# Kernel tuning notes

Measured on AMD Instinct MI355X. Metric: run time of the kernel, lower is better.

The kernel has to match this reference:

```python
import jax, jax.numpy as jnp
import numpy as np

NMS_THR = 0.7
TOPK = 128      # fixed post-NMS rois per level (static padding for jit)
OUT = 14        # RoIAlign output size
SAMPLES = 2     # samples per bin per dim (fixed approximation of sampling_ratio=-1)
STRIDES = (32.0, 16.0, 8.0)


def get_channel(a):
    # a: [..., 4] boxes as (cx, cy, w, h); FPN level assignment, clamped to [1, 4]
    s = jnp.sqrt(a[..., 2] * a[..., 3])
    return jnp.clip(jnp.floor(3.0 + jnp.log2(s / 224.0)), 1.0, 4.0)


def cxcywh_to_xyxy(b):
    cx, cy, w, h = b[..., 0], b[..., 1], b[..., 2], b[..., 3]
    return jnp.stack([cx - w / 2, cy - h / 2, cx + w / 2, cy + h / 2], axis=-1)


def pairwise_iou(b):
    x1, y1, x2, y2 = b[:, 0], b[:, 1], b[:, 2], b[:, 3]
    area = jnp.maximum(x2 - x1, 0.0) * jnp.maximum(y2 - y1, 0.0)
    ix1 = jnp.maximum(x1[:, None], x1[None, :])
    iy1 = jnp.maximum(y1[:, None], y1[None, :])
    ix2 = jnp.minimum(x2[:, None], x2[None, :])
    iy2 = jnp.minimum(y2[:, None], y2[None, :])
    inter = jnp.maximum(ix2 - ix1, 0.0) * jnp.maximum(iy2 - iy1, 0.0)
    union = area[:, None] + area[None, :] - inter
    return inter / jnp.maximum(union, 1e-9)


def nms_keep(boxes_xyxy, scores, thr):
    # Greedy NMS over masked scores (-inf entries sort last and are excluded later).
    n = scores.shape[0]
    order = jnp.argsort(-scores)
    iou = pairwise_iou(boxes_xyxy[order])  # [N, N]
    idx = jnp.arange(n)

    def body(sup, i):
        keep_i = ~sup[i]
        sup = sup | (keep_i & (iou[i] > thr) & (idx > i))
        return sup, keep_i

    _, keeps_sorted = jax.lax.scan(body, jnp.zeros(n, dtype=bool), idx)
    return jnp.zeros(n, dtype=bool).at[order].set(keeps_sorted)


def roi_align(feat, boxes):
    # feat: [C, H, W]; boxes: [K, 4]. NOTE: the original prepare_boxes feeds
    # (cx, cy, w, h) straight into RoIAlign, which interprets them as
    # (x1, y1, x2, y2) -- replicated faithfully here. spatial_scale = 1.
    C, H, W = feat.shape
    K = boxes.shape[0]
    x1, y1, x2, y2 = boxes[:, 0], boxes[:, 1], boxes[:, 2], boxes[:, 3]
    rw = jnp.maximum(x2 - x1, 1.0)
    rh = jnp.maximum(y2 - y1, 1.0)
    bw = rw / OUT
    bh = rh / OUT
    # fractional bin offsets, [OUT*SAMPLES]
    f = (jnp.arange(OUT, dtype=feat.dtype)[:, None]
         + (jnp.arange(SAMPLES, dtype=feat.dtype)[None, :] + 0.5) / SAMPLES).reshape(-1)
    ys = y1[:, None] + bh[:, None] * f[None, :]  # [K, S]
    xs = x1[:, None] + bw[:, None] * f[None, :]
    Y = ys[:, :, None]  # [K, S, 1]
    X = xs[:, None, :]  # [K, 1, S]
    valid = (Y > -1.0) & (Y < H) & (X > -1.0) & (X < W)  # [K, S, S]
    Yc = jnp.clip(Y, 0.0, H - 1.0)
    Xc = jnp.clip(X, 0.0, W - 1.0)
    y0 = jnp.floor(Yc)
    x0 = jnp.floor(Xc)
    y0i = y0.astype(jnp.int32)
    x0i = x0.astype(jnp.int32)
    y1i = jnp.minimum(y0i + 1, H - 1)
    x1i = jnp.minimum(x0i + 1, W - 1)
    ly = Yc - y0
    lx = Xc - x0
    hy = 1.0 - ly
    hx = 1.0 - lx
    g = lambda yi, xi: feat[:, yi, xi]  # -> [C, K, S, S]
    val = (g(y0i, x0i) * (hy * hx) + g(y0i, x1i) * (hy * lx)
           + g(y1i, x0i) * (ly * hx) + g(y1i, x1i) * (ly * lx))
    val = val * valid.astype(val.dtype)
    val = val.reshape(C, K, OUT, SAMPLES, OUT, SAMPLES).mean(axis=(3, 5))
    return jnp.transpose(val, (1, 0, 2, 3))  # [K, C, OUT, OUT]


def level_extract(feat, boxes, scores, levs, nl):
    # one image, one target FPN level: mask, NMS, fixed top-K select, RoIAlign
    mask = levs == nl
    msc = jnp.where(mask, scores, -jnp.inf)
    xyxy = cxcywh_to_xyxy(boxes)
    keep = nms_keep(jax.lax.stop_gradient(xyxy), jax.lax.stop_gradient(msc), NMS_THR)
    eff = jnp.where(keep & mask, msc, -jnp.inf)
    vals, sel = jax.lax.top_k(jax.lax.stop_gradient(eff), TOPK)
    valid = jnp.isfinite(vals)
    rois = boxes[sel] * valid[:, None].astype(boxes.dtype)
    out = roi_align(feat, rois)
    return out * valid[:, None, None, None].astype(out.dtype)


def _forward(p32, p16, p8, p4, a32, a16, a8, s32, s16, s8):
    anchors = (a32, a16, a8)  # p4 proposals are computed then discarded in the
    # original (grouping loop only runs l in range(3)); p4 features are never
    # RoIAligned either (nl loops 1..3), so p4 only appears as an unused input.
    levs = jnp.concatenate([get_channel(a) for a in anchors], axis=1)      # [B, N]
    boxes = jnp.concatenate([a * s for a, s in zip(anchors, STRIDES)], axis=1)
    scores = jnp.concatenate([s32, s16, s8], axis=1)
    outs = []
    for nl, feat in zip((1.0, 2.0, 3.0), (p32, p16, p8)):
        fn = jax.vmap(lambda f, b, s, l, nl=nl: level_extract(f, b, s, l, nl))
        outs.append(fn(feat, boxes, scores, levs))  # [B, TOPK, C, 14, 14]
    return jnp.concatenate(outs, axis=1)  # [B, 3*TOPK, C, 14, 14]


def setup_inputs():
    key = jax.random.key(0)
    ks = jax.random.split(key, 10)
    B, C = 2, 256
    p32 = jax.random.normal(ks[0], (B, C, 32, 32), jnp.float32)
    p16 = jax.random.normal(ks[1], (B, C, 64, 64), jnp.float32)
    p8 = jax.random.normal(ks[2], (B, C, 128, 128), jnp.float32)
    p4 = jax.random.normal(ks[3], (B, C, 256, 256), jnp.float32)

    def mk_anchors(k, n, hf):
        k1, k2 = jax.random.split(k)
        cxy = jax.random.uniform(k1, (B, n, 2), jnp.float32) * hf
        wh = 16.0 + jax.random.uniform(k2, (B, n, 2), jnp.float32) * 434.0
        return jnp.concatenate([cxy, wh], axis=-1)

    anchors_32 = mk_anchors(ks[4], 512, 32.0)
    anchors_16 = mk_anchors(ks[5], 1024, 64.0)
    anchors_8 = mk_anchors(ks[6], 2048, 128.0)
    scores_32 = jax.random.normal(ks[7], (B, 512), jnp.float32)
    scores_16 = jax.random.normal(ks[8], (B, 1024), jnp.float32)
    scores_8 = jax.random.normal(ks[9], (B, 2048), jnp.float32)
    return dict(p32=p32, p16=p16, p8=p8, p4=p4,
                anchors_32=anchors_32, anchors_16=anchors_16, anchors_8=anchors_8,
                scores_32=scores_32, scores_16=scores_16, scores_8=scores_8)


def reference(p32, p16, p8, p4, anchors_32, anchors_16, anchors_8,
              scores_32, scores_16, scores_8):
    return _forward(p32, p16, p8, p4, anchors_32, anchors_16, anchors_8,
                    scores_32, scores_16, scores_8)
```

## Files before the change

### kernel.cpp

```cpp
#include <hip/hip_runtime.h>
#include <stdint.h>

#define NMS_THR 0.7f
#define TOPK 128
#define NTOT 3584
#define CAP 2048
#define CHUNK 256
#define OUTSZ 14
#define NSAMP 28

typedef unsigned long long u64;
typedef float vf4 __attribute__((ext_vector_type(4)));
typedef float float2u __attribute__((ext_vector_type(2), aligned(4)));

__device__ __forceinline__ u64 shfl_xor64(u64 v, int mask) {
    int lo = __shfl_xor((int)(unsigned)v, mask);
    int hi = __shfl_xor((int)(v >> 32), mask);
    return ((u64)(unsigned)hi << 32) | (unsigned)lo;
}
__device__ __forceinline__ void cex_shfl(u64 &e, int t, int j, int k) {
    u64 p = shfl_xor64(e, j);
    bool up = ((t & k) == 0);
    bool lower = ((t & j) == 0);
    u64 mn = (e < p) ? e : p;
    u64 mx = (e < p) ? p : e;
    e = (lower == up) ? mn : mx;
}
__device__ __forceinline__ float boxarea(float4 b) {
    return __fmul_rn(fmaxf(__fsub_rn(b.z, b.x), 0.0f),
                     fmaxf(__fsub_rn(b.w, b.y), 0.0f));
}
__device__ __forceinline__ bool iou_gt(float4 a, float aa, float4 b, float ba) {
    float i1 = fmaxf(a.x, b.x), i2 = fmaxf(a.y, b.y);
    float i3 = fminf(a.z, b.z), i4 = fminf(a.w, b.w);
    float inr = __fmul_rn(fmaxf(__fsub_rn(i3, i1), 0.0f),
                          fmaxf(__fsub_rn(i4, i2), 0.0f));
    float unr = __fsub_rn(__fadd_rn(aa, ba), inr);
    return __fdiv_rn(inr, fmaxf(unr, 1e-9f)) > NMS_THR;
}

__device__ __forceinline__ void fetch_anchor(
    const float* __restrict__ a32, const float* __restrict__ a16,
    const float* __restrict__ a8,
    const float* __restrict__ s32, const float* __restrict__ s16,
    const float* __restrict__ s8,
    int b, int i, float* A, float* st, float* sc)
{
    const float* P;
    if (i < 512) {
        P = a32 + (b * 512 + i) * 4;  *st = 32.0f; *sc = s32[b * 512 + i];
    } else if (i < 1536) {
        int j = i - 512;
        P = a16 + (b * 1024 + j) * 4; *st = 16.0f; *sc = s16[b * 1024 + j];
    } else {
        int j = i - 1536;
        P = a8 + (b * 2048 + j) * 4;  *st = 8.0f;  *sc = s8[b * 2048 + j];
    }
    float4 v = *(const float4*)P;
    A[0] = v.x; A[1] = v.y; A[2] = v.z; A[3] = v.w;
}

__global__ __launch_bounds__(1024) void select_kernel(
    const float* __restrict__ a32, const float* __restrict__ a16,
    const float* __restrict__ a8,
    const float* __restrict__ s32, const float* __restrict__ s16,
    const float* __restrict__ s8,
    float* __restrict__ rois,
    int* __restrict__ validOut)
{
    __shared__ u64 keys[CAP];
    __shared__ float4 cbox4[CAP];
    __shared__ float4 kb4[TOPK];
    __shared__ float karea[TOPK];
    __shared__ u64 extw[16];
    __shared__ int selList[TOPK];
    __shared__ int mCount, keptSh;

    int prob = blockIdx.x;
    int b = prob / 3;
    int nl = prob % 3 + 1;
    int tid = threadIdx.x;
    int lane = tid & 63;
    int wv = tid >> 6;
    int t0 = (wv << 7) + lane;
    int t1 = t0 + 64;

    if (tid == 0) mCount = 0;
    __syncthreads();

    for (int i = tid; i < NTOT; i += 1024) {
        float A[4], st, sc;
        fetch_anchor(a32, a16, a8, s32, s16, s8, b, i, A, &st, &sc);
        float s = sqrtf(__fmul_rn(A[2], A[3]));
        float lv = floorf(__fadd_rn(3.0f, log2f(__fdiv_rn(s, 224.0f))));
        lv = fminf(fmaxf(lv, 1.0f), 4.0f);
        bool sel = ((int)lv == nl);
        u64 bal = __ballot(sel);
        if (bal) {
            int pos0;
            if (lane == 0) pos0 = atomicAdd(&mCount, __popcll(bal));
            pos0 = __shfl(pos0, 0);
            if (sel) {
                unsigned u = __float_as_uint(sc);
                u = (u & 0x80000000u) ? ~u : (u | 0x80000000u);
                unsigned d = ~u;
                int pos = pos0 + __popcll(bal & ((1ull << lane) - 1ull));
                if (pos < CAP) keys[pos] = ((u64)d << 32) | (unsigned)i;
            }
        }
    }
    __syncthreads();
    int m = mCount;
    if (m > CAP) m = CAP;
    for (int i = m + tid; i < CAP; i += 1024) keys[i] = ~0ull;
    __syncthreads();

    {
        u64 e0 = keys[t0], e1 = keys[t1];
        for (int k = 2; k <= 128; k <<= 1) {
            int jstart = k >> 1;
            if (k == 128) {
                bool up = ((t0 & k) == 0);
                if ((e0 > e1) == up) { u64 tmp = e0; e0 = e1; e1 = tmp; }
                jstart = 32;
            }
            for (int j = jstart; j > 0; j >>= 1) {
                cex_shfl(e0, t0, j, k);
                cex_shfl(e1, t1, j, k);
            }
        }
        keys[t0] = e0; keys[t1] = e1;
    }
    __syncthreads();
    for (int k = 256; k <= 2048; k <<= 1) {
        for (int j = k >> 1; j >= 128; j >>= 1) {
            for (int t = tid; t < CAP; t += 1024) {
                int ixj = t ^ j;
                if (ixj > t) {
                    u64 a = keys[t], bb = keys[ixj];
                    bool up = ((t & k) == 0);
                    if ((a > bb) == up) { keys[t] = bb; keys[ixj] = a; }
                }
            }
            __syncthreads();
        }
        {
            u64 e0 = keys[t0], e1 = keys[t1];
            bool up = ((t0 & k) == 0);
            if ((e0 > e1) == up) { u64 tmp = e0; e0 = e1; e1 = tmp; }
            for (int j = 32; j > 0; j >>= 1) {
                cex_shfl(e0, t0, j, k);
                cex_shfl(e1, t1, j, k);
            }
            keys[t0] = e0; keys[t1] = e1;
        }
        __syncthreads();
    }

    for (int r = tid; r < m; r += 1024) {
        int orig = (int)(keys[r] & 0xffffffffu);
        float A[4], st, sc;
        fetch_anchor(a32, a16, a8, s32, s16, s8, b, orig, A, &st, &sc);
        float cx = A[0] * st, cy = A[1] * st, w = A[2] * st, h = A[3] * st;
        float4 v;
        v.x = __fsub_rn(cx, 0.5f * w);
        v.y = __fsub_rn(cy, 0.5f * h);
        v.z = __fadd_rn(cx, 0.5f * w);
        v.w = __fadd_rn(cy, 0.5f * h);
        cbox4[r] = v;
    }
    __syncthreads();

    int kept = 0;
    int g = wv & 3;
    int ksub = wv >> 2;
    for (int base = 0; base < m && kept < TOPK; base += CHUNK) {
        int n = m - base; if (n > CHUNK) n = CHUNK;

        int c = g * 64 + lane;
        bool cv = c < n;
        float4 cb = cbox4[base + (cv ? c : 0)];
        float car = boxarea(cb);
        bool s = false;
        for (int kk = ksub; kk < kept; kk += 4) {
            if (iou_gt(kb4[kk], karea[kk], cb, car)) s = true;
        }
        u64 bal = __ballot(s && cv);
        if (lane == 0) extw[wv] = bal;
        __syncthreads();

        if (wv == 0) {
            u64 e0 = extw[0] | extw[4] | extw[8]  | extw[12];
            u64 e1 = extw[1] | extw[5] | extw[9]  | extw[13];
            u64 e2 = extw[2] | extw[6] | extw[10] | extw[14];
            u64 e3 = extw[3] | extw[7] | extw[11] | extw[15];
            int c0 = lane, c1 = 64 + lane, c2 = 128 + lane, c3 = 192 + lane;
            float4 B0 = cbox4[base + (c0 < n ? c0 : 0)];
            float4 B1 = cbox4[base + (c1 < n ? c1 : 0)];
            float4 B2 = cbox4[base + (c2 < n ? c2 : 0)];
            float4 B3 = cbox4[base + (c3 < n ? c3 : 0)];
            float a0 = boxarea(B0), a1 = boxarea(B1);
            float a2 = boxarea(B2), a3 = boxarea(B3);
            bool al0 = (c0 < n) && !((e0 >> lane) & 1ull);
            bool al1 = (c1 < n) && !((e1 >> lane) & 1ull);
            bool al2 = (c2 < n) && !((e2 >> lane) & 1ull);
            bool al3 = (c3 < n) && !((e3 >> lane) & 1ull);
            int nk = kept;
            while (nk < TOPK) {
                u64 b0 = __ballot(al0);
                u64 b1 = __ballot(al1);
                u64 b2 = __ballot(al2);
                u64 b3 = __ballot(al3);
                int j;
                if (b0)      j = __builtin_ctzll(b0);
                else if (b1) j = 64 + __builtin_ctzll(b1);
                else if (b2) j = 128 + __builtin_ctzll(b2);
                else if (b3) j = 192 + __builtin_ctzll(b3);
                else break;
                float4 pb = cbox4[base + j];
                float par = boxarea(pb);
                if (lane == 0) {
                    selList[nk] = base + j;
                    kb4[nk] = pb; karea[nk] = par;
                }
                al0 = al0 && (c0 != j) && !((c0 > j) && iou_gt(pb, par, B0, a0));
                al1 = al1 && (c1 != j) && !((c1 > j) && iou_gt(pb, par, B1, a1));
                al2 = al2 && (c2 != j) && !((c2 > j) && iou_gt(pb, par, B2, a2));
                al3 = al3 && (c3 != j) && !((c3 > j) && iou_gt(pb, par, B3, a3));
                nk++;
            }
            if (lane == 0) keptSh = nk;
        }
        __syncthreads();
        kept = keptSh;
    }

    for (int k = tid; k < TOPK; k += 1024) {
        float4 rv = make_float4(0.0f, 0.0f, 0.0f, 0.0f);
        int vld = 0;
        if (k < kept) {
            int orig = (int)(keys[selList[k]] & 0xffffffffu);
            float A[4], st, sc;
            fetch_anchor(a32, a16, a8, s32, s16, s8, b, orig, A, &st, &sc);
            rv = make_float4(A[0] * st, A[1] * st, A[2] * st, A[3] * st);
            vld = 1;
        }
        ((float4*)rois)[prob * TOPK + k] = rv;
        validOut[prob * TOPK + k] = vld;
    }
}

__global__ __launch_bounds__(256) void roialign_kernel(
    const float* __restrict__ p32, const float* __restrict__ p16,
    const float* __restrict__ p8,
    const float* __restrict__ rois, const int* __restrict__ validIn,
    float* __restrict__ out)
{
    int roiIdx = blockIdx.x;
    int b = roiIdx / 384;
    int slot = roiIdx - b * 384;
    int lvl = slot / TOPK;
    int k = slot - lvl * TOPK;
    int prob = b * 3 + lvl;
    int tid = threadIdx.x;

    int vld = validIn[prob * TOPK + k];
    if (!vld) return;

    float* O = out + (size_t)roiIdx * 256 * 196;

    int W;
    const float* feat;
    if (lvl == 0)      { W = 32;  feat = p32; }
    else if (lvl == 1) { W = 64;  feat = p16; }
    else               { W = 128; feat = p8; }
    int HW = W * W;
    const float* F0 = feat + (size_t)b * 256 * HW;

    __shared__ int sxb[NSAMP], sy0[NSAMP], sy1[NSAMP];
    __shared__ float swx0[NSAMP], swx1[NSAMP], shy[NSAMP], sly[NSAMP];
    __shared__ int sxv[NSAMP], syv[NSAMP];
    __shared__ int oiL[OUTSZ], ojL[OUTSZ];
    __shared__ int nyx[2];

    if (tid < 2 * NSAMP) {
        const float* R = rois + ((size_t)prob * TOPK + k) * 4;
        float x1 = R[0], y1 = R[1], x2 = R[2], y2 = R[3];
        float rw = fmaxf(__fsub_rn(x2, x1), 1.0f);
        float rh = fmaxf(__fsub_rn(y2, y1), 1.0f);
        float bw = __fdiv_rn(rw, 14.0f);
        float bh = __fdiv_rn(rh, 14.0f);
        int axis = tid / NSAMP;
        int s = tid - axis * NSAMP;
        float fi = (float)(s >> 1) + ((s & 1) ? 0.75f : 0.25f);
        float start = axis ? y1 : x1;
        float bsz = axis ? bh : bw;
        float lim = (float)W;
        float X = __fadd_rn(start, __fmul_rn(bsz, fi));
        bool v = (X > -1.0f) && (X < lim);
        float Xc = fminf(fmaxf(X, 0.0f), lim - 1.0f);
        float x0f = floorf(Xc);
        int x0 = (int)x0f;
        float l = __fsub_rn(Xc, x0f);
        float hh = __fsub_rn(1.0f, l);
        float vf = v ? 1.0f : 0.0f;
        if (axis == 0) {
            int base; float w0, w1;
            if (x0 >= W - 1) { base = W - 2; w0 = 0.0f; w1 = vf; }
            else             { base = x0;    w0 = hh * vf; w1 = l * vf; }
            sxb[s] = base; swx0[s] = w0; swx1[s] = w1; sxv[s] = v ? 1 : 0;
        } else {
            sy0[s] = x0; sy1[s] = min(x0 + 1, W - 1);
            shy[s] = hh * vf; sly[s] = l * vf; syv[s] = v ? 1 : 0;
        }
    }
    __syncthreads();

    if (tid == 0) {
        int n = 0;
        for (int oi = 0; oi < OUTSZ; oi++)
            if (syv[2 * oi] | syv[2 * oi + 1]) oiL[n++] = oi;
        nyx[0] = n;
    }
    if (tid == 1) {
        int n = 0;
        for (int oj = 0; oj < OUTSZ; oj++)
            if (sxv[2 * oj] | sxv[2 * oj + 1]) ojL[n++] = oj;
        nyx[1] = n;
    }
    __syncthreads();

    int ny = nyx[0], nx = nyx[1];
    int total = ny * nx;
    if (total == 0) return;

    int w = tid >> 6;
    int lane = tid & 63;

    for (int ci = w; ci < total; ci += 4) {
        int oi = oiL[ci / nx];
        int oj = ojL[ci - (ci / nx) * nx];
        int sA = oi * 2, sB = sA + 1;
        int tA = oj * 2, tB = tA + 1;
        int y0A = sy0[sA], y1A = sy1[sA], y0B = sy0[sB], y1B = sy1[sB];
        float hyA = shy[sA], lyA = sly[sA], hyB = shy[sB], lyB = sly[sB];
        int xA = sxb[tA], xB = sxb[tB];
        float xw0A = swx0[tA], xw1A = swx1[tA];
        float xw0B = swx0[tB], xw1B = swx1[tB];
        int p = oi * 14 + oj;

        for (int it = 0; it < 4; it++) {
            int c = lane + it * 64;
            const float* F = F0 + c * HW;
            const float* rA0 = F + y0A * W;
            const float* rA1 = F + y1A * W;
            const float* rB0 = F + y0B * W;
            const float* rB1 = F + y1B * W;

            float2u a0 = *(const float2u*)(rA0 + xA);
            float2u a1 = *(const float2u*)(rA1 + xA);
            float2u c0 = *(const float2u*)(rA0 + xB);
            float2u c1 = *(const float2u*)(rA1 + xB);
            float2u b0 = *(const float2u*)(rB0 + xA);
            float2u b1 = *(const float2u*)(rB1 + xA);
            float2u d0 = *(const float2u*)(rB0 + xB);
            float2u d1 = *(const float2u*)(rB1 + xB);

            float s00 = hyA * (xw0A * a0.x + xw1A * a0.y) + lyA * (xw0A * a1.x + xw1A * a1.y);
            float s01 = hyA * (xw0B * c0.x + xw1B * c0.y) + lyA * (xw0B * c1.x + xw1B * c1.y);
            float s10 = hyB * (xw0A * b0.x + xw1A * b0.y) + lyB * (xw0A * b1.x + xw1A * b1.y);
            float s11 = hyB * (xw0B * d0.x + xw1B * d0.y) + lyB * (xw0B * d1.x + xw1B * d1.y);
            O[c * 196 + p] = 0.25f * (s00 + s01 + s10 + s11);
        }
    }
}

extern "C" void kernel_launch(void* const* d_in, const int* in_sizes, int n_in,
                              void* d_out, int out_size, void* d_ws, size_t ws_size,
                              hipStream_t stream) {
    const float* p32 = (const float*)d_in[0];
    const float* p16 = (const float*)d_in[1];
    const float* p8  = (const float*)d_in[2];
    const float* a32 = (const float*)d_in[4];
    const float* a16 = (const float*)d_in[5];
    const float* a8  = (const float*)d_in[6];
    const float* s32 = (const float*)d_in[7];
    const float* s16 = (const float*)d_in[8];
    const float* s8  = (const float*)d_in[9];
    float* out = (float*)d_out;

    const size_t totalFloats = 3072 + 768;

    float* base;
    if (ws_size >= totalFloats * 4) {
        base = (float*)d_ws;
    } else {
        base = (float*)d_in[3];
    }
    float* rois  = base;
    int*   valid = (int*)(base + 3072);

    hipMemsetAsync(out, 0, out_size, stream);
    select_kernel<<<6, 1024, 0, stream>>>(a32, a16, a8, s32, s16, s8,
                                          rois, valid);
    roialign_kernel<<<768, 256, 0, stream>>>(p32, p16, p8, rois, valid, out);
}
```

Before: 359.9 us.

## Split select into prep and NMS kernels, shrink NMS chunks, fold zeroing into RoIAlign

Result: no change. 358.8 us (-0.3%).

```diff
diff --git a/kernel.cpp b/kernel.cpp
--- a/kernel.cpp
+++ b/kernel.cpp
@@ -5,7 +5,6 @@
 #define TOPK 128
 #define NTOT 3584
 #define CAP 2048
-#define CHUNK 256
 #define OUTSZ 14
 #define NSAMP 28
 
@@ -25,6 +24,10 @@
     u64 mn = (e < p) ? e : p;
     u64 mx = (e < p) ? p : e;
     e = (lower == up) ? mn : mx;
+}
+__device__ __forceinline__ void cex_reg(u64 &a, u64 &b, int t, int k) {
+    bool up = ((t & k) == 0);
+    if ((a > b) == up) { u64 x = a; a = b; b = x; }
 }
 __device__ __forceinline__ float boxarea(float4 b) {
     return __fmul_rn(fmaxf(__fsub_rn(b.z, b.x), 0.0f),
@@ -60,21 +63,17 @@
     A[0] = v.x; A[1] = v.y; A[2] = v.z; A[3] = v.w;
 }
 
-__global__ __launch_bounds__(1024) void select_kernel(
+__global__ __launch_bounds__(1024) void prep_kernel(
     const float* __restrict__ a32, const float* __restrict__ a16,
     const float* __restrict__ a8,
     const float* __restrict__ s32, const float* __restrict__ s16,
     const float* __restrict__ s8,
-    float* __restrict__ rois,
-    int* __restrict__ validOut)
+    int* __restrict__ sidxG,
+    float4* __restrict__ cboxG,
+    int* __restrict__ mG)
 {
     __shared__ u64 keys[CAP];
-    __shared__ float4 cbox4[CAP];
-    __shared__ float4 kb4[TOPK];
-    __shared__ float karea[TOPK];
-    __shared__ u64 extw[16];
-    __shared__ int selList[TOPK];
-    __shared__ int mCount, keptSh;
+    __shared__ int mCount;
 
     int prob = blockIdx.x;
     int b = prob / 3;
@@ -120,8 +119,7 @@
         for (int k = 2; k <= 128; k <<= 1) {
             int jstart = k >> 1;
             if (k == 128) {
-                bool up = ((t0 & k) == 0);
-                if ((e0 > e1) == up) { u64 tmp = e0; e0 = e1; e1 = tmp; }
+                cex_reg(e0, e1, t0, k);
                 jstart = 32;
             }
             for (int j = jstart; j > 0; j >>= 1) {
@@ -146,8 +144,7 @@
         }
         {
             u64 e0 = keys[t0], e1 = keys[t1];
-            bool up = ((t0 & k) == 0);
-            if ((e0 > e1) == up) { u64 tmp = e0; e0 = e1; e1 = tmp; }
+            cex_reg(e0, e1, t0, k);
             for (int j = 32; j > 0; j >>= 1) {
                 cex_shfl(e0, t0, j, k);
                 cex_shfl(e1, t1, j, k);
@@ -159,6 +156,7 @@
 
     for (int r = tid; r < m; r += 1024) {
         int orig = (int)(keys[r] & 0xffffffffu);
+        sidxG[prob * CAP + r] = orig;
         float A[4], st, sc;
         fetch_anchor(a32, a16, a8, s32, s16, s8, b, orig, A, &st, &sc);
         float cx = A[0] * st, cy = A[1] * st, w = A[2] * st, h = A[3] * st;
@@ -167,66 +165,71 @@
         v.y = __fsub_rn(cy, 0.5f * h);
         v.z = __fadd_rn(cx, 0.5f * w);
         v.w = __fadd_rn(cy, 0.5f * h);
-        cbox4[r] = v;
-    }
+        cboxG[prob * CAP + r] = v;
+    }
+    if (tid == 0) mG[prob] = m;
+}
+
+__global__ __launch_bounds__(1024) void nms_kernel(
+    const float4* __restrict__ cboxG, const int* __restrict__ sidxG,
+    const int* __restrict__ mG,
+    const float* __restrict__ a32, const float* __restrict__ a16,
+    const float* __restrict__ a8,
+    const float* __restrict__ s32, const float* __restrict__ s16,
+    const float* __restrict__ s8,
+    float* __restrict__ rois,
+    int* __restrict__ validOut)
+{
+    __shared__ float4 kb4[TOPK];
+    __shared__ float karea[TOPK];
+    __shared__ u64 extw[16];
+    __shared__ int selList[TOPK];
+    __shared__ int keptSh;
+
+    int prob = blockIdx.x;
+    int b = prob / 3;
+    int tid = threadIdx.x;
+    int lane = tid & 63;
+    int wv = tid >> 6;
+    int m = mG[prob];
+
+    if (tid == 0) keptSh = 0;
     __syncthreads();
 
     int kept = 0;
-    int g = wv & 3;
-    int ksub = wv >> 2;
-    for (int base = 0; base < m && kept < TOPK; base += CHUNK) {
-        int n = m - base; if (n > CHUNK) n = CHUNK;
-
-        int c = g * 64 + lane;
-        bool cv = c < n;
-        float4 cb = cbox4[base + (cv ? c : 0)];
+    for (int base = 0; base < m && kept < TOPK; base += 64) {
+        int n = m - base; if (n > 64) n = 64;
+        bool cv = lane < n;
+        float4 cb = cboxG[prob * CAP + base + (cv ? lane : 0)];
         float car = boxarea(cb);
+
         bool s = false;
-        for (int kk = ksub; kk < kept; kk += 4) {
+        for (int kk = wv; kk < kept; kk += 16)
             if (iou_gt(kb4[kk], karea[kk], cb, car)) s = true;
-        }
-        u64 bal = __ballot(s && cv);
-        if (lane == 0) extw[wv] = bal;
+        u64 balA = __ballot(s && cv);
+        if (lane == 0) extw[wv] = balA;
         __syncthreads();
 
         if (wv == 0) {
-            u64 e0 = extw[0] | extw[4] | extw[8]  | extw[12];
-            u64 e1 = extw[1] | extw[5] | extw[9]  | extw[13];
-            u64 e2 = extw[2] | extw[6] | extw[10] | extw[14];
-            u64 e3 = extw[3] | extw[7] | extw[11] | extw[15];
-            int c0 = lane, c1 = 64 + lane, c2 = 128 + lane, c3 = 192 + lane;
-            float4 B0 = cbox4[base + (c0 < n ? c0 : 0)];
-            float4 B1 = cbox4[base + (c1 < n ? c1 : 0)];
-            float4 B2 = cbox4[base + (c2 < n ? c2 : 0)];
-            float4 B3 = cbox4[base + (c3 < n ? c3 : 0)];
-            float a0 = boxarea(B0), a1 = boxarea(B1);
-            float a2 = boxarea(B2), a3 = boxarea(B3);
-            bool al0 = (c0 < n) && !((e0 >> lane) & 1ull);
-            bool al1 = (c1 < n) && !((e1 >> lane) & 1ull);
-            bool al2 = (c2 < n) && !((e2 >> lane) & 1ull);
-            bool al3 = (c3 < n) && !((e3 >> lane) & 1ull);
+            u64 ext = extw[0] | extw[1] | extw[2]  | extw[3]
+                    | extw[4] | extw[5] | extw[6]  | extw[7]
+                    | extw[8] | extw[9] | extw[10] | extw[11]
+                    | extw[12]| extw[13]| extw[14] | extw[15];
+            bool alive = cv && !((ext >> lane) & 1ull);
             int nk = kept;
             while (nk < TOPK) {
-                u64 b0 = __ballot(al0);
-                u64 b1 = __ballot(al1);
-                u64 b2 = __ballot(al2);
-                u64 b3 = __ballot(al3);
-                int j;
-                if (b0)      j = __builtin_ctzll(b0);
-                else if (b1) j = 64 + __builtin_ctzll(b1);
-                else if (b2) j = 128 + __builtin_ctzll(b2);
-                else if (b3) j = 192 + __builtin_ctzll(b3);
-                else break;
-                float4 pb = cbox4[base + j];
-                float par = boxarea(pb);
-                if (lane == 0) {
-                    selList[nk] = base + j;
-                    kb4[nk] = pb; karea[nk] = par;
-                }
-                al0 = al0 && (c0 != j) && !((c0 > j) && iou_gt(pb, par, B0, a0));
-                al1 = al1 && (c1 != j) && !((c1 > j) && iou_gt(pb, par, B1, a1));
-                al2 = al2 && (c2 != j) && !((c2 > j) && iou_gt(pb, par, B2, a2));
-                al3 = al3 && (c3 != j) && !((c3 > j) && iou_gt(pb, par, B3, a3));
+                u64 bal = __ballot(alive);
+                if (bal == 0ull) break;
+                int pick = __builtin_ctzll(bal);
+                float4 pb;
+                pb.x = __shfl(cb.x, pick);
+                pb.y = __shfl(cb.y, pick);
+                pb.z = __shfl(cb.z, pick);
+                pb.w = __shfl(cb.w, pick);
+                float par = __shfl(car, pick);
+                if (lane == 0) selList[nk] = base + pick;
+                if (lane == 1) { kb4[nk] = pb; karea[nk] = par; }
+                alive = alive && (lane != pick) && !iou_gt(pb, par, cb, car);
                 nk++;
             }
             if (lane == 0) keptSh = nk;
@@ -239,7 +242,7 @@
         float4 rv = make_float4(0.0f, 0.0f, 0.0f, 0.0f);
         int vld = 0;
         if (k < kept) {
-            int orig = (int)(keys[selList[k]] & 0xffffffffu);
+            int orig = sidxG[prob * CAP + selList[k]];
             float A[4], st, sc;
             fetch_anchor(a32, a16, a8, s32, s16, s8, b, orig, A, &st, &sc);
             rv = make_float4(A[0] * st, A[1] * st, A[2] * st, A[3] * st);
@@ -264,10 +267,14 @@
     int prob = b * 3 + lvl;
     int tid = threadIdx.x;
 
+    float* O = out + (size_t)roiIdx * 256 * 196;
+
+    vf4 z = (vf4)0.0f;
+    vf4* O4 = (vf4*)O;
+    for (int i = tid; i < 12544; i += 256) O4[i] = z;
+
     int vld = validIn[prob * TOPK + k];
     if (!vld) return;
-
-    float* O = out + (size_t)roiIdx * 256 * 196;
 
     int W;
     const float* feat;
@@ -389,7 +396,11 @@
     const float* s8  = (const float*)d_in[9];
     float* out = (float*)d_out;
 
-    const size_t totalFloats = 3072 + 768;
+    const size_t offValid = 3072;
+    const size_t offMArr  = offValid + 768;
+    const size_t offSidx  = offMArr + 8;
+    const size_t offCbox  = offSidx + 6 * CAP;
+    const size_t totalFloats = offCbox + (size_t)6 * CAP * 4;
 
     float* base;
     if (ws_size >= totalFloats * 4) {
@@ -397,11 +408,16 @@
     } else {
         base = (float*)d_in[3];
     }
-    float* rois  = base;
-    int*   valid = (int*)(base + 3072);
-
-    hipMemsetAsync(out, 0, out_size, stream);
-    select_kernel<<<6, 1024, 0, stream>>>(a32, a16, a8, s32, s16, s8,
-                                          rois, valid);
+    float*  rois  = base;
+    int*    valid = (int*)(base + offValid);
+    int*    mArr  = (int*)(base + offMArr);
+    int*    sidx  = (int*)(base + offSidx);
+    float4* cbox  = (float4*)(base + offCbox);
+
+    prep_kernel<<<6, 1024, 0, stream>>>(a32, a16, a8, s32, s16, s8,
+                                        sidx, cbox, mArr);
+    nms_kernel<<<6, 1024, 0, stream>>>(cbox, sidx, mArr,
+                                       a32, a16, a8, s32, s16, s8,
+                                       rois, valid);
     roialign_kernel<<<768, 256, 0, stream>>>(p32, p16, p8, rois, valid, out);
 }
```
